# Kernel tuning notes

Measured on AMD Instinct MI355X. Metric: run time of the kernel, lower is better.

## Reference

```python
import jax, jax.numpy as jnp
import numpy as np

N_NODES = 50000
N_EDGES = 500000
IN_DIM = 128
HIDDEN = 32
HEADS = 8
OUT_DIM = HIDDEN * HEADS  # 256
NEG_SLOPE = 0.2


def setup_inputs() -> dict:
    key = jax.random.key(0)
    ks = jax.random.split(key, 10)
    s = lambda fan: 1.0 / np.sqrt(fan)
    x = jax.random.normal(ks[0], (N_NODES, IN_DIM), dtype=jnp.float32)
    edge_index = jax.random.randint(ks[1], (2, N_EDGES), 0, N_NODES, dtype=jnp.int32)
    W1 = jax.random.normal(ks[2], (IN_DIM, HEADS * HIDDEN), jnp.float32) * s(IN_DIM)
    a_src1 = jax.random.normal(ks[3], (HEADS, HIDDEN), jnp.float32) * s(HIDDEN)
    a_dst1 = jax.random.normal(ks[4], (HEADS, HIDDEN), jnp.float32) * s(HIDDEN)
    b1 = jnp.zeros((HEADS * HIDDEN,), jnp.float32)
    W2 = jax.random.normal(ks[5], (OUT_DIM, OUT_DIM), jnp.float32) * s(OUT_DIM)
    a_src2 = jax.random.normal(ks[6], (1, OUT_DIM), jnp.float32) * s(OUT_DIM)
    a_dst2 = jax.random.normal(ks[7], (1, OUT_DIM), jnp.float32) * s(OUT_DIM)
    b2 = jnp.zeros((OUT_DIM,), jnp.float32)
    return {"x": x, "edge_index": edge_index, "W1": W1, "a_src1": a_src1,
            "a_dst1": a_dst1, "b1": b1, "W2": W2, "a_src2": a_src2,
            "a_dst2": a_dst2, "b2": b2}


def _gat_layer(x, src, dst, W, a_src, a_dst, b, heads, ch, concat):
    N = x.shape[0]
    h = (x @ W).reshape(N, heads, ch)                      # [N,H,C]
    e_src = jnp.sum(h * a_src[None], axis=-1)              # [N,H]
    e_dst = jnp.sum(h * a_dst[None], axis=-1)              # [N,H]
    e = jax.nn.leaky_relu(e_src[src] + e_dst[dst], NEG_SLOPE)  # [E,H]
    # softmax over incoming edges of each destination node
    m = jax.ops.segment_max(e, dst, num_segments=N)        # [N,H]
    e = jnp.exp(e - m[dst])
    denom = jax.ops.segment_sum(e, dst, num_segments=N)    # [N,H]
    alpha = e / (denom[dst] + 1e-16)                       # [E,H]
    msg = h[src] * alpha[:, :, None]                       # [E,H,C]
    out = jax.ops.segment_sum(msg, dst, num_segments=N)    # [N,H,C]
    out = out.reshape(N, heads * ch) if concat else out.mean(axis=1)
    return out + b


def reference(x, edge_index, W1, a_src1, a_dst1, b1, W2, a_src2, a_dst2, b2):
    N = x.shape[0]
    # add self loops (PyG GATConv default)
    loops = jnp.arange(N, dtype=edge_index.dtype)
    src = jnp.concatenate([edge_index[0], loops])
    dst = jnp.concatenate([edge_index[1], loops])
    # dropout is identity in eval mode
    h = _gat_layer(x, src, dst, W1, a_src1, a_dst1, b1, HEADS, HIDDEN, True)
    h = jax.nn.elu(h)
    out = _gat_layer(h, src, dst, W2, a_src2, a_dst2, b2, 1, OUT_DIM, False)
    return out
```

## Files before the change

kernel.cpp:

```cpp
#include <hip/hip_runtime.h>
#include <math.h>

#define N_NODES 50000
#define E_ORIG  500000
#define E_TOT   550000
#define NB      196

typedef _Float16 half8 __attribute__((ext_vector_type(8)));
typedef _Float16 half4 __attribute__((ext_vector_type(4)));
typedef float    v4f   __attribute__((ext_vector_type(4)));

__global__ void k_count(const int* __restrict__ ei, int* __restrict__ deg) {
    int e = blockIdx.x * blockDim.x + threadIdx.x;
    if (e >= E_TOT) return;
    int d = (e < E_ORIG) ? ei[E_ORIG + e] : (e - E_ORIG);
    atomicAdd(&deg[d], 1);
}

__global__ __launch_bounds__(256) void k_blocksum(const int* __restrict__ deg,
                                                  int* __restrict__ bsum) {
    int t = threadIdx.x;
    int i = blockIdx.x * 256 + t;
    int v = (i < N_NODES) ? deg[i] : 0;
#pragma unroll
    for (int mk = 1; mk < 64; mk <<= 1) v += __shfl_xor(v, mk, 64);
    __shared__ int ws[4];
    if ((t & 63) == 0) ws[t >> 6] = v;
    __syncthreads();
    if (t == 0) bsum[blockIdx.x] = ws[0] + ws[1] + ws[2] + ws[3];
}

__global__ __launch_bounds__(256) void k_scanbsum(const int* __restrict__ bsum,
                                                  int* __restrict__ boff) {
    __shared__ int s[256];
    int t = threadIdx.x;
    int v = (t < NB) ? bsum[t] : 0;
    s[t] = v;
    __syncthreads();
    for (int o = 1; o < 256; o <<= 1) {
        int x = (t >= o) ? s[t - o] : 0;
        __syncthreads();
        s[t] += x;
        __syncthreads();
    }
    if (t <= NB) boff[t] = (t == 0) ? 0 : s[t - 1];
}

__global__ __launch_bounds__(256) void k_offsets(const int* __restrict__ deg,
                                                 const int* __restrict__ boff,
                                                 int* __restrict__ offsets,
                                                 int* __restrict__ cur) {
    __shared__ int s[256];
    int t = threadIdx.x;
    int i = blockIdx.x * 256 + t;
    int v = (i < N_NODES) ? deg[i] : 0;
    s[t] = v;
    __syncthreads();
    for (int o = 1; o < 256; o <<= 1) {
        int x = (t >= o) ? s[t - o] : 0;
        __syncthreads();
        s[t] += x;
        __syncthreads();
    }
    int off = boff[blockIdx.x] + s[t] - v;
    if (i <= N_NODES) {
        offsets[i] = off;
        if (i < N_NODES) cur[i] = off;
    }
}

__global__ void k_scatter(const int* __restrict__ ei, int* __restrict__ cur,
                          int* __restrict__ csr_src, int* __restrict__ csr_dst) {
    int e = blockIdx.x * blockDim.x + threadIdx.x;
    if (e >= E_TOT) return;
    int s, d;
    if (e < E_ORIG) { s = ei[e]; d = ei[E_ORIG + e]; }
    else            { s = e - E_ORIG; d = s; }
    int slot = atomicAdd(&cur[d], 1);
    csr_src[slot] = s;
    csr_dst[slot] = d;
}

__global__ void k_prepw(const float* __restrict__ W1, const float* __restrict__ W2,
                        const float* __restrict__ as2, const float* __restrict__ ad2,
                        _Float16* __restrict__ w1t, _Float16* __restrict__ w2t,
                        float* __restrict__ vs2, float* __restrict__ vd2,
                        int* __restrict__ deg) {
    int i = blockIdx.x * blockDim.x + threadIdx.x;
    if (i < 128 * 256) {
        int k = i >> 8, c = i & 255;
        w1t[(size_t)c * 128 + k] = (_Float16)W1[i];
        return;
    }
    int j = i - 128 * 256;
    if (j < 256 * 256) {
        int k = j >> 8, c = j & 255;
        w2t[(size_t)c * 256 + k] = (_Float16)W2[j];
        return;
    }
    j -= 256 * 256;
    if (j < 256) {
        float s = 0.f, d = 0.f;
        for (int c = 0; c < 256; c++) {
            float w = W2[(size_t)j * 256 + c];
            s += w * as2[c];
            d += w * ad2[c];
        }
        vs2[j] = s;
        vd2[j] = d;
        return;
    }
    j -= 256;
    if (j < N_NODES) deg[j] = 0;
}

__global__ __launch_bounds__(256) void k_wts1(
    const int* __restrict__ csr_src, const int* __restrict__ csr_dst,
    const float* __restrict__ es, const float* __restrict__ ed,
    float* __restrict__ w1w) {
    int i = blockIdx.x * blockDim.x + threadIdx.x;
    if (i >= E_TOT * 8) return;
    int e = i >> 3, h = i & 7;
    int s = csr_src[e], d = csr_dst[e];
    float l = es[(size_t)s * 8 + h] + ed[(size_t)d * 8 + h];
    l = l > 0.f ? l : 0.2f * l;
    w1w[i] = __expf(l);
}

__global__ __launch_bounds__(256) void k_wts2(
    const int* __restrict__ csr_src, const int* __restrict__ csr_dst,
    const float* __restrict__ es2, const float* __restrict__ ed2,
    float* __restrict__ w2w) {
    int e = blockIdx.x * blockDim.x + threadIdx.x;
    if (e >= E_TOT) return;
    float l = es2[csr_src[e]] + ed2[csr_dst[e]];
    l = l > 0.f ? l : 0.2f * l;
    w2w[e] = __expf(l);
}

__global__ __launch_bounds__(256) void k_gemm1(
    const float* __restrict__ X, const _Float16* __restrict__ Bt,
    const float* __restrict__ a_s, const float* __restrict__ a_d,
    _Float16* __restrict__ H, float* __restrict__ es, float* __restrict__ ed) {
    int t = threadIdx.x, w = t >> 6, lane = t & 63;
    int quad = lane >> 4, l16 = lane & 15;
    int row0 = blockIdx.x * 32;
    int colbase = w * 64;

    v4f acc[2][4];
#pragma unroll
    for (int i = 0; i < 2; i++)
#pragma unroll
        for (int j = 0; j < 4; j++) acc[i][j] = (v4f){0.f, 0.f, 0.f, 0.f};

    int r0 = row0 + l16;      if (r0 >= N_NODES) r0 = N_NODES - 1;
    int r1 = row0 + 16 + l16; if (r1 >= N_NODES) r1 = N_NODES - 1;
    const float4* a0p = (const float4*)(X + (size_t)r0 * 128) + quad * 2;
    const float4* a1p = (const float4*)(X + (size_t)r1 * 128) + quad * 2;
    const half8* bp[4];
#pragma unroll
    for (int ct = 0; ct < 4; ct++)
        bp[ct] = (const half8*)(Bt + (size_t)(colbase + ct * 16 + l16) * 128 + quad * 8);

#pragma unroll
    for (int kc = 0; kc < 4; kc++) {
        float4 f0 = a0p[kc * 8], f1 = a0p[kc * 8 + 1];
        float4 f2 = a1p[kc * 8], f3 = a1p[kc * 8 + 1];
        half8 av0 = (half8){(_Float16)f0.x, (_Float16)f0.y, (_Float16)f0.z, (_Float16)f0.w,
                            (_Float16)f1.x, (_Float16)f1.y, (_Float16)f1.z, (_Float16)f1.w};
        half8 av1 = (half8){(_Float16)f2.x, (_Float16)f2.y, (_Float16)f2.z, (_Float16)f2.w,
                            (_Float16)f3.x, (_Float16)f3.y, (_Float16)f3.z, (_Float16)f3.w};
#pragma unroll
        for (int ct = 0; ct < 4; ct++) {
            half8 bv = bp[ct][kc * 4];
            acc[0][ct] = __builtin_amdgcn_mfma_f32_16x16x32_f16(av0, bv, acc[0][ct], 0, 0, 0);
            acc[1][ct] = __builtin_amdgcn_mfma_f32_16x16x32_f16(av1, bv, acc[1][ct], 0, 0, 0);
        }
    }

    float asv[4], adv[4];
#pragma unroll
    for (int ct = 0; ct < 4; ct++) {
        asv[ct] = a_s[colbase + ct * 16 + l16];
        adv[ct] = a_d[colbase + ct * 16 + l16];
    }
#pragma unroll
    for (int rt = 0; rt < 2; rt++) {
#pragma unroll
        for (int hp = 0; hp < 2; hp++) {
#pragma unroll
            for (int reg = 0; reg < 4; reg++) {
                float ps = acc[rt][2 * hp][reg] * asv[2 * hp] +
                           acc[rt][2 * hp + 1][reg] * asv[2 * hp + 1];
                float pd = acc[rt][2 * hp][reg] * adv[2 * hp] +
                           acc[rt][2 * hp + 1][reg] * adv[2 * hp + 1];
#pragma unroll
                for (int mk = 1; mk < 16; mk <<= 1) {
                    ps += __shfl_xor(ps, mk, 64);
                    pd += __shfl_xor(pd, mk, 64);
                }
                if (l16 == 0) {
                    int row = row0 + rt * 16 + quad * 4 + reg;
                    if (row < N_NODES) {
                        int head = w * 2 + hp;
                        es[(size_t)row * 8 + head] = ps;
                        ed[(size_t)row * 8 + head] = pd;
                    }
                }
            }
        }
    }

    __shared__ _Float16 SH[32][264];
#pragma unroll
    for (int rt = 0; rt < 2; rt++)
#pragma unroll
        for (int ct = 0; ct < 4; ct++)
#pragma unroll
            for (int reg = 0; reg < 4; reg++)
                SH[rt * 16 + quad * 4 + reg][colbase + ct * 16 + l16] =
                    (_Float16)acc[rt][ct][reg];
    __syncthreads();
#pragma unroll
    for (int j = 0; j < 4; j++) {
        int c = j * 256 + t;
        int row = c >> 5, col8 = c & 31;
        int gr = row0 + row;
        if (gr < N_NODES)
            *(half8*)(H + (size_t)gr * 256 + col8 * 8) = *(const half8*)&SH[row][col8 * 8];
    }
}

__global__ __launch_bounds__(256) void k_gemm2(
    const _Float16* __restrict__ A, const _Float16* __restrict__ Bt,
    const float* __restrict__ bias, float* __restrict__ OUT) {
    int t = threadIdx.x, w = t >> 6, lane = t & 63;
    int quad = lane >> 4, l16 = lane & 15;
    int row0 = blockIdx.x * 32;
    int colbase = w * 64;

    v4f acc[2][4];
#pragma unroll
    for (int i = 0; i < 2; i++)
#pragma unroll
        for (int j = 0; j < 4; j++) acc[i][j] = (v4f){0.f, 0.f, 0.f, 0.f};

    int r0 = row0 + l16;      if (r0 >= N_NODES) r0 = N_NODES - 1;
    int r1 = row0 + 16 + l16; if (r1 >= N_NODES) r1 = N_NODES - 1;
    const half8* a0 = (const half8*)(A + (size_t)r0 * 256 + quad * 8);
    const half8* a1 = (const half8*)(A + (size_t)r1 * 256 + quad * 8);
    const half8* bp[4];
#pragma unroll
    for (int ct = 0; ct < 4; ct++)
        bp[ct] = (const half8*)(Bt + (size_t)(colbase + ct * 16 + l16) * 256 + quad * 8);

#pragma unroll
    for (int kc = 0; kc < 8; kc++) {
        half8 av0 = a0[kc * 4];
        half8 av1 = a1[kc * 4];
#pragma unroll
        for (int ct = 0; ct < 4; ct++) {
            half8 bv = bp[ct][kc * 4];
            acc[0][ct] = __builtin_amdgcn_mfma_f32_16x16x32_f16(av0, bv, acc[0][ct], 0, 0, 0);
            acc[1][ct] = __builtin_amdgcn_mfma_f32_16x16x32_f16(av1, bv, acc[1][ct], 0, 0, 0);
        }
    }

    __shared__ float SF[32][260];
#pragma unroll
    for (int rt = 0; rt < 2; rt++)
#pragma unroll
        for (int ct = 0; ct < 4; ct++)
#pragma unroll
            for (int reg = 0; reg < 4; reg++)
                SF[rt * 16 + quad * 4 + reg][colbase + ct * 16 + l16] = acc[rt][ct][reg];
    __syncthreads();
#pragma unroll
    for (int j = 0; j < 8; j++) {
        int c = j * 256 + t;
        int row = c >> 6, c4 = c & 63;
        int gr = row0 + row;
        if (gr < N_NODES) {
            float4 v = *(const float4*)&SF[row][c4 * 4];
            float4 bb = ((const float4*)bias)[c4];
            float4 o = make_float4(v.x + bb.x, v.y + bb.y, v.z + bb.z, v.w + bb.w);
            *(float4*)(OUT + (size_t)gr * 256 + c4 * 4) = o;
        }
    }
}

__global__ __launch_bounds__(256) void k_agg1(
    const _Float16* __restrict__ H1, const float* __restrict__ w1w,
    const int* __restrict__ offsets, const int* __restrict__ csr_src,
    const float* __restrict__ b1, const float* __restrict__ vs2,
    const float* __restrict__ vd2, _Float16* __restrict__ out1,
    float* __restrict__ es2, float* __restrict__ ed2) {
    int t = threadIdx.x, w = t >> 6, lane = t & 63;
    int n = blockIdx.x * 4 + w;
    int hB = lane >> 3;
    int beg = offsets[n];
    int deg = offsets[n + 1] - beg;

    const char* __restrict__ Hb = (const char*)H1 + lane * 8;
    const float* __restrict__ pw = w1w + (size_t)beg * 8 + hB;
    float a0 = 0.f, a1 = 0.f, a2 = 0.f, a3 = 0.f, den = 0.f;

    for (int base = 0; base < deg; base += 64) {
        int rem = deg - base; if (rem > 64) rem = 64;
        int idx = beg + base + lane;
        if (idx >= E_TOT) idx = E_TOT - 1;
        int sreg = csr_src[idx];
        int i = 0;
        for (; i + 1 < rem; i += 2) {
            int s0 = __shfl(sreg, i);
            int s1 = __shfl(sreg, i + 1);
            float w0 = pw[(base + i) * 8];
            float w1 = pw[(base + i + 1) * 8];
            half4 h0 = *(const half4*)(Hb + ((unsigned)s0 << 9));
            half4 h1 = *(const half4*)(Hb + ((unsigned)s1 << 9));
            a0 += w0 * (float)h0[0]; a1 += w0 * (float)h0[1];
            a2 += w0 * (float)h0[2]; a3 += w0 * (float)h0[3];
            a0 += w1 * (float)h1[0]; a1 += w1 * (float)h1[1];
            a2 += w1 * (float)h1[2]; a3 += w1 * (float)h1[3];
            den += w0 + w1;
        }
        if (i < rem) {
            int s0 = __shfl(sreg, i);
            float w0 = pw[(base + i) * 8];
            half4 h0 = *(const half4*)(Hb + ((unsigned)s0 << 9));
            a0 += w0 * (float)h0[0]; a1 += w0 * (float)h0[1];
            a2 += w0 * (float)h0[2]; a3 += w0 * (float)h0[3];
            den += w0;
        }
    }

    float r = 1.f / (den + 1e-16f);
    float4 bb = ((const float4*)b1)[lane];
    float o0 = a0 * r + bb.x, o1 = a1 * r + bb.y;
    float o2 = a2 * r + bb.z, o3 = a3 * r + bb.w;
    o0 = o0 > 0.f ? o0 : __expf(o0) - 1.f;
    o1 = o1 > 0.f ? o1 : __expf(o1) - 1.f;
    o2 = o2 > 0.f ? o2 : __expf(o2) - 1.f;
    o3 = o3 > 0.f ? o3 : __expf(o3) - 1.f;
    ((half4*)(out1 + (size_t)n * 256))[lane] =
        (half4){(_Float16)o0, (_Float16)o1, (_Float16)o2, (_Float16)o3};

    float4 vs = ((const float4*)vs2)[lane];
    float4 vd = ((const float4*)vd2)[lane];
    float ps = o0 * vs.x + o1 * vs.y + o2 * vs.z + o3 * vs.w;
    float pd = o0 * vd.x + o1 * vd.y + o2 * vd.z + o3 * vd.w;
#pragma unroll
    for (int mk = 1; mk < 64; mk <<= 1) {
        ps += __shfl_xor(ps, mk, 64);
        pd += __shfl_xor(pd, mk, 64);
    }
    if (lane == 0) { es2[n] = ps; ed2[n] = pd; }
}

__global__ __launch_bounds__(256) void k_agg2(
    const _Float16* __restrict__ O1, const float* __restrict__ w2w,
    const int* __restrict__ offsets, const int* __restrict__ csr_src,
    _Float16* __restrict__ xagg) {
    int t = threadIdx.x, w = t >> 6, lane = t & 63;
    int n = blockIdx.x * 4 + w;
    int beg = offsets[n];
    int deg = offsets[n + 1] - beg;

    const char* __restrict__ Ob = (const char*)O1 + lane * 8;
    float a0 = 0.f, a1 = 0.f, a2 = 0.f, a3 = 0.f, den = 0.f;

    for (int base = 0; base < deg; base += 64) {
        int rem = deg - base; if (rem > 64) rem = 64;
        int idx = beg + base + lane;
        if (idx >= E_TOT) idx = E_TOT - 1;
        int sreg = csr_src[idx];
        float wreg = w2w[idx];
        int i = 0;
        for (; i + 1 < rem; i += 2) {
            int s0 = __shfl(sreg, i);
            int s1 = __shfl(sreg, i + 1);
            float w0 = __shfl(wreg, i);
            float w1 = __shfl(wreg, i + 1);
            half4 h0 = *(const half4*)(Ob + ((unsigned)s0 << 9));
            half4 h1 = *(const half4*)(Ob + ((unsigned)s1 << 9));
            a0 += w0 * (float)h0[0]; a1 += w0 * (float)h0[1];
            a2 += w0 * (float)h0[2]; a3 += w0 * (float)h0[3];
            a0 += w1 * (float)h1[0]; a1 += w1 * (float)h1[1];
            a2 += w1 * (float)h1[2]; a3 += w1 * (float)h1[3];
            den += w0 + w1;
        }
        if (i < rem) {
            int s0 = __shfl(sreg, i);
            float w0 = __shfl(wreg, i);
            half4 h0 = *(const half4*)(Ob + ((unsigned)s0 << 9));
            a0 += w0 * (float)h0[0]; a1 += w0 * (float)h0[1];
            a2 += w0 * (float)h0[2]; a3 += w0 * (float)h0[3];
            den += w0;
        }
    }

    float r = 1.f / (den + 1e-16f);
    ((half4*)(xagg + (size_t)n * 256))[lane] =
        (half4){(_Float16)(a0 * r), (_Float16)(a1 * r),
                (_Float16)(a2 * r), (_Float16)(a3 * r)};
}

extern "C" void kernel_launch(void* const* d_in, const int* in_sizes, int n_in,
                              void* d_out, int out_size, void* d_ws, size_t ws_size,
                              hipStream_t stream) {
    const float* x   = (const float*)d_in[0];
    const int*   ei  = (const int*)d_in[1];
    const float* W1  = (const float*)d_in[2];
    const float* as1 = (const float*)d_in[3];
    const float* ad1 = (const float*)d_in[4];
    const float* b1  = (const float*)d_in[5];
    const float* W2  = (const float*)d_in[6];
    const float* as2 = (const float*)d_in[7];
    const float* ad2 = (const float*)d_in[8];
    const float* b2  = (const float*)d_in[9];
    float* out = (float*)d_out;

    char* ws = (char*)d_ws;
    size_t off = 0;
    auto alloc = [&](size_t bytes) {
        void* p = ws + off;
        off = (off + bytes + 255) & ~(size_t)255;
        return p;
    };
    _Float16* h1h     = (_Float16*)alloc((size_t)N_NODES * 256 * 2);
    _Float16* out1h   = (_Float16*)alloc((size_t)N_NODES * 256 * 2);
    _Float16* xagg    = (_Float16*)alloc((size_t)N_NODES * 256 * 2);
    _Float16* w1t     = (_Float16*)alloc((size_t)128 * 256 * 2);
    _Float16* w2t     = (_Float16*)alloc((size_t)256 * 256 * 2);
    float*    es1     = (float*)alloc((size_t)N_NODES * 8 * 4);
    float*    ed1     = (float*)alloc((size_t)N_NODES * 8 * 4);
    float*    es2     = (float*)alloc((size_t)N_NODES * 4);
    float*    ed2     = (float*)alloc((size_t)N_NODES * 4);
    float*    vs2     = (float*)alloc(256 * 4);
    float*    vd2     = (float*)alloc(256 * 4);
    float*    w1w     = (float*)alloc((size_t)E_TOT * 8 * 4);
    float*    w2w     = (float*)alloc((size_t)E_TOT * 4);
    int*      deg     = (int*)alloc((size_t)N_NODES * 4);
    int*      offsets = (int*)alloc((size_t)(N_NODES + 1) * 4);
    int*      cur     = (int*)alloc((size_t)N_NODES * 4);
    int*      csr_src = (int*)alloc((size_t)E_TOT * 4);
    int*      csr_dst = (int*)alloc((size_t)E_TOT * 4);
    int*      bsum    = (int*)alloc((size_t)NB * 4);
    int*      boff    = (int*)alloc((size_t)(NB + 1) * 4);

    const int TB = 256;
    int gridE = (E_TOT + TB - 1) / TB;
    int gridG = (N_NODES + 31) / 32;
    int gridA = N_NODES / 4;

    int prepN = 128 * 256 + 256 * 256 + 256 + N_NODES;
    k_prepw<<<(prepN + TB - 1) / TB, TB, 0, stream>>>(W1, W2, as2, ad2,
                                                      w1t, w2t, vs2, vd2, deg);
    k_count<<<gridE, TB, 0, stream>>>(ei, deg);
    k_blocksum<<<NB, TB, 0, stream>>>(deg, bsum);
    k_scanbsum<<<1, TB, 0, stream>>>(bsum, boff);
    k_offsets<<<NB, TB, 0, stream>>>(deg, boff, offsets, cur);
    k_scatter<<<gridE, TB, 0, stream>>>(ei, cur, csr_src, csr_dst);

    k_gemm1<<<gridG, TB, 0, stream>>>(x, w1t, as1, ad1, h1h, es1, ed1);
    k_wts1<<<(E_TOT * 8 + TB - 1) / TB, TB, 0, stream>>>(csr_src, csr_dst,
                                                         es1, ed1, w1w);
    k_agg1<<<gridA, TB, 0, stream>>>(h1h, w1w, offsets, csr_src, b1,
                                     vs2, vd2, out1h, es2, ed2);

    k_wts2<<<gridE, TB, 0, stream>>>(csr_src, csr_dst, es2, ed2, w2w);
    k_agg2<<<gridA, TB, 0, stream>>>(out1h, w2w, offsets, csr_src, xagg);
    k_gemm2<<<gridG, TB, 0, stream>>>(xagg, w2t, b2, out);
}
```

Measured before the change: 339.4 us.

## Split wavefront into half-waves gathering 16-byte rows in aggregation kernels

The two aggregation kernels now split each wavefront into two 32-lane halves that handle alternate edges. Each lane loads 8 halfs (16 bytes) per neighbor instead of 4, and the two halves' partial sums are combined with a cross-half shuffle at the end. This aims for wider loads and two independent gathers in flight per wave. The GEMM epilogues also stage the output through a 16-row shared buffer in two passes, which halves shared memory use at the cost of an extra barrier.

```diff
diff --git a/kernel.cpp b/kernel.cpp
--- a/kernel.cpp
+++ b/kernel.cpp
@@ -211,23 +211,24 @@
         }
     }
 
-    __shared__ _Float16 SH[32][264];
-#pragma unroll
-    for (int rt = 0; rt < 2; rt++)
+    __shared__ _Float16 SH[16][264];
+#pragma unroll
+    for (int rt = 0; rt < 2; rt++) {
+        if (rt) __syncthreads();
 #pragma unroll
         for (int ct = 0; ct < 4; ct++)
 #pragma unroll
             for (int reg = 0; reg < 4; reg++)
-                SH[rt * 16 + quad * 4 + reg][colbase + ct * 16 + l16] =
-                    (_Float16)acc[rt][ct][reg];
-    __syncthreads();
-#pragma unroll
-    for (int j = 0; j < 4; j++) {
-        int c = j * 256 + t;
-        int row = c >> 5, col8 = c & 31;
-        int gr = row0 + row;
-        if (gr < N_NODES)
-            *(half8*)(H + (size_t)gr * 256 + col8 * 8) = *(const half8*)&SH[row][col8 * 8];
+                SH[quad * 4 + reg][colbase + ct * 16 + l16] = (_Float16)acc[rt][ct][reg];
+        __syncthreads();
+#pragma unroll
+        for (int j = 0; j < 2; j++) {
+            int c = j * 256 + t;
+            int row = c >> 5, col8 = c & 31;
+            int gr = row0 + rt * 16 + row;
+            if (gr < N_NODES)
+                *(half8*)(H + (size_t)gr * 256 + col8 * 8) = *(const half8*)&SH[row][col8 * 8];
+        }
     }
 }
 
@@ -266,25 +267,27 @@
         }
     }
 
-    __shared__ float SF[32][260];
-#pragma unroll
-    for (int rt = 0; rt < 2; rt++)
+    __shared__ float SF[16][260];
+#pragma unroll
+    for (int rt = 0; rt < 2; rt++) {
+        if (rt) __syncthreads();
 #pragma unroll
         for (int ct = 0; ct < 4; ct++)
 #pragma unroll
             for (int reg = 0; reg < 4; reg++)
-                SF[rt * 16 + quad * 4 + reg][colbase + ct * 16 + l16] = acc[rt][ct][reg];
-    __syncthreads();
-#pragma unroll
-    for (int j = 0; j < 8; j++) {
-        int c = j * 256 + t;
-        int row = c >> 6, c4 = c & 63;
-        int gr = row0 + row;
-        if (gr < N_NODES) {
-            float4 v = *(const float4*)&SF[row][c4 * 4];
-            float4 bb = ((const float4*)bias)[c4];
-            float4 o = make_float4(v.x + bb.x, v.y + bb.y, v.z + bb.z, v.w + bb.w);
-            *(float4*)(OUT + (size_t)gr * 256 + c4 * 4) = o;
+                SF[quad * 4 + reg][colbase + ct * 16 + l16] = acc[rt][ct][reg];
+        __syncthreads();
+#pragma unroll
+        for (int j = 0; j < 4; j++) {
+            int c = j * 256 + t;
+            int row = c >> 6, c4 = c & 63;
+            int gr = row0 + rt * 16 + row;
+            if (gr < N_NODES) {
+                float4 v = *(const float4*)&SF[row][c4 * 4];
+                float4 bb = ((const float4*)bias)[c4];
+                float4 o = make_float4(v.x + bb.x, v.y + bb.y, v.z + bb.z, v.w + bb.w);
+                *(float4*)(OUT + (size_t)gr * 256 + c4 * 4) = o;
+            }
         }
     }
 }
@@ -297,60 +300,71 @@
     float* __restrict__ es2, float* __restrict__ ed2) {
     int t = threadIdx.x, w = t >> 6, lane = t & 63;
     int n = blockIdx.x * 4 + w;
-    int hB = lane >> 3;
+    int half = lane >> 5;
+    int c8 = lane & 31;
+    int hB = c8 >> 2;
     int beg = offsets[n];
     int deg = offsets[n + 1] - beg;
 
-    const char* __restrict__ Hb = (const char*)H1 + lane * 8;
+    const char* __restrict__ Hb = (const char*)H1 + c8 * 16;
     const float* __restrict__ pw = w1w + (size_t)beg * 8 + hB;
-    float a0 = 0.f, a1 = 0.f, a2 = 0.f, a3 = 0.f, den = 0.f;
+    float a0 = 0.f, a1 = 0.f, a2 = 0.f, a3 = 0.f;
+    float a4 = 0.f, a5 = 0.f, a6 = 0.f, a7 = 0.f, den = 0.f;
 
     for (int base = 0; base < deg; base += 64) {
         int rem = deg - base; if (rem > 64) rem = 64;
         int idx = beg + base + lane;
         if (idx >= E_TOT) idx = E_TOT - 1;
         int sreg = csr_src[idx];
-        int i = 0;
-        for (; i + 1 < rem; i += 2) {
-            int s0 = __shfl(sreg, i);
-            int s1 = __shfl(sreg, i + 1);
-            float w0 = pw[(base + i) * 8];
-            float w1 = pw[(base + i + 1) * 8];
-            half4 h0 = *(const half4*)(Hb + ((unsigned)s0 << 9));
-            half4 h1 = *(const half4*)(Hb + ((unsigned)s1 << 9));
-            a0 += w0 * (float)h0[0]; a1 += w0 * (float)h0[1];
-            a2 += w0 * (float)h0[2]; a3 += w0 * (float)h0[3];
-            a0 += w1 * (float)h1[0]; a1 += w1 * (float)h1[1];
-            a2 += w1 * (float)h1[2]; a3 += w1 * (float)h1[3];
-            den += w0 + w1;
-        }
-        if (i < rem) {
+        for (int i = half; i < rem; i += 2) {
             int s0 = __shfl(sreg, i);
             float w0 = pw[(base + i) * 8];
-            half4 h0 = *(const half4*)(Hb + ((unsigned)s0 << 9));
-            a0 += w0 * (float)h0[0]; a1 += w0 * (float)h0[1];
-            a2 += w0 * (float)h0[2]; a3 += w0 * (float)h0[3];
+            half8 h = *(const half8*)(Hb + ((size_t)(unsigned)s0 << 9));
+            a0 += w0 * (float)h[0]; a1 += w0 * (float)h[1];
+            a2 += w0 * (float)h[2]; a3 += w0 * (float)h[3];
+            a4 += w0 * (float)h[4]; a5 += w0 * (float)h[5];
+            a6 += w0 * (float)h[6]; a7 += w0 * (float)h[7];
             den += w0;
         }
     }
 
+    a0 += __shfl_xor(a0, 32, 64); a1 += __shfl_xor(a1, 32, 64);
+    a2 += __shfl_xor(a2, 32, 64); a3 += __shfl_xor(a3, 32, 64);
+    a4 += __shfl_xor(a4, 32, 64); a5 += __shfl_xor(a5, 32, 64);
+    a6 += __shfl_xor(a6, 32, 64); a7 += __shfl_xor(a7, 32, 64);
+    den += __shfl_xor(den, 32, 64);
+
     float r = 1.f / (den + 1e-16f);
-    float4 bb = ((const float4*)b1)[lane];
-    float o0 = a0 * r + bb.x, o1 = a1 * r + bb.y;
-    float o2 = a2 * r + bb.z, o3 = a3 * r + bb.w;
+    float4 bl = ((const float4*)b1)[c8 * 2];
+    float4 bh = ((const float4*)b1)[c8 * 2 + 1];
+    float o0 = a0 * r + bl.x, o1 = a1 * r + bl.y;
+    float o2 = a2 * r + bl.z, o3 = a3 * r + bl.w;
+    float o4 = a4 * r + bh.x, o5 = a5 * r + bh.y;
+    float o6 = a6 * r + bh.z, o7 = a7 * r + bh.w;
     o0 = o0 > 0.f ? o0 : __expf(o0) - 1.f;
     o1 = o1 > 0.f ? o1 : __expf(o1) - 1.f;
     o2 = o2 > 0.f ? o2 : __expf(o2) - 1.f;
     o3 = o3 > 0.f ? o3 : __expf(o3) - 1.f;
-    ((half4*)(out1 + (size_t)n * 256))[lane] =
-        (half4){(_Float16)o0, (_Float16)o1, (_Float16)o2, (_Float16)o3};
-
-    float4 vs = ((const float4*)vs2)[lane];
-    float4 vd = ((const float4*)vd2)[lane];
-    float ps = o0 * vs.x + o1 * vs.y + o2 * vs.z + o3 * vs.w;
-    float pd = o0 * vd.x + o1 * vd.y + o2 * vd.z + o3 * vd.w;
-#pragma unroll
-    for (int mk = 1; mk < 64; mk <<= 1) {
+    o4 = o4 > 0.f ? o4 : __expf(o4) - 1.f;
+    o5 = o5 > 0.f ? o5 : __expf(o5) - 1.f;
+    o6 = o6 > 0.f ? o6 : __expf(o6) - 1.f;
+    o7 = o7 > 0.f ? o7 : __expf(o7) - 1.f;
+    if (half == 0) {
+        half8 hv = (half8){(_Float16)o0, (_Float16)o1, (_Float16)o2, (_Float16)o3,
+                           (_Float16)o4, (_Float16)o5, (_Float16)o6, (_Float16)o7};
+        *((half8*)(out1 + (size_t)n * 256) + c8) = hv;
+    }
+
+    float4 vsl = ((const float4*)vs2)[c8 * 2];
+    float4 vsh = ((const float4*)vs2)[c8 * 2 + 1];
+    float4 vdl = ((const float4*)vd2)[c8 * 2];
+    float4 vdh = ((const float4*)vd2)[c8 * 2 + 1];
+    float ps = o0 * vsl.x + o1 * vsl.y + o2 * vsl.z + o3 * vsl.w +
+               o4 * vsh.x + o5 * vsh.y + o6 * vsh.z + o7 * vsh.w;
+    float pd = o0 * vdl.x + o1 * vdl.y + o2 * vdl.z + o3 * vdl.w +
+               o4 * vdh.x + o5 * vdh.y + o6 * vdh.z + o7 * vdh.w;
+#pragma unroll
+    for (int mk = 1; mk < 32; mk <<= 1) {
         ps += __shfl_xor(ps, mk, 64);
         pd += __shfl_xor(pd, mk, 64);
     }
@@ -363,11 +377,13 @@
     _Float16* __restrict__ xagg) {
     int t = threadIdx.x, w = t >> 6, lane = t & 63;
     int n = blockIdx.x * 4 + w;
+    int half = lane >> 5, c8 = lane & 31;
     int beg = offsets[n];
     int deg = offsets[n + 1] - beg;
 
-    const char* __restrict__ Ob = (const char*)O1 + lane * 8;
-    float a0 = 0.f, a1 = 0.f, a2 = 0.f, a3 = 0.f, den = 0.f;
+    const char* __restrict__ Ob = (const char*)O1 + c8 * 16;
+    float a0 = 0.f, a1 = 0.f, a2 = 0.f, a3 = 0.f;
+    float a4 = 0.f, a5 = 0.f, a6 = 0.f, a7 = 0.f, den = 0.f;
 
     for (int base = 0; base < deg; base += 64) {
         int rem = deg - base; if (rem > 64) rem = 64;
@@ -375,34 +391,32 @@
         if (idx >= E_TOT) idx = E_TOT - 1;
         int sreg = csr_src[idx];
         float wreg = w2w[idx];
-        int i = 0;
-        for (; i + 1 < rem; i += 2) {
-            int s0 = __shfl(sreg, i);
-            int s1 = __shfl(sreg, i + 1);
-            float w0 = __shfl(wreg, i);
-            float w1 = __shfl(wreg, i + 1);
-            half4 h0 = *(const half4*)(Ob + ((unsigned)s0 << 9));
-            half4 h1 = *(const half4*)(Ob + ((unsigned)s1 << 9));
-            a0 += w0 * (float)h0[0]; a1 += w0 * (float)h0[1];
-            a2 += w0 * (float)h0[2]; a3 += w0 * (float)h0[3];
-            a0 += w1 * (float)h1[0]; a1 += w1 * (float)h1[1];
-            a2 += w1 * (float)h1[2]; a3 += w1 * (float)h1[3];
-            den += w0 + w1;
-        }
-        if (i < rem) {
+        for (int i = half; i < rem; i += 2) {
             int s0 = __shfl(sreg, i);
             float w0 = __shfl(wreg, i);
-            half4 h0 = *(const half4*)(Ob + ((unsigned)s0 << 9));
-            a0 += w0 * (float)h0[0]; a1 += w0 * (float)h0[1];
-            a2 += w0 * (float)h0[2]; a3 += w0 * (float)h0[3];
+            half8 h = *(const half8*)(Ob + ((size_t)(unsigned)s0 << 9));
+            a0 += w0 * (float)h[0]; a1 += w0 * (float)h[1];
+            a2 += w0 * (float)h[2]; a3 += w0 * (float)h[3];
+            a4 += w0 * (float)h[4]; a5 += w0 * (float)h[5];
+            a6 += w0 * (float)h[6]; a7 += w0 * (float)h[7];
             den += w0;
         }
     }
 
+    a0 += __shfl_xor(a0, 32, 64); a1 += __shfl_xor(a1, 32, 64);
+    a2 += __shfl_xor(a2, 32, 64); a3 += __shfl_xor(a3, 32, 64);
+    a4 += __shfl_xor(a4, 32, 64); a5 += __shfl_xor(a5, 32, 64);
+    a6 += __shfl_xor(a6, 32, 64); a7 += __shfl_xor(a7, 32, 64);
+    den += __shfl_xor(den, 32, 64);
+
     float r = 1.f / (den + 1e-16f);
-    ((half4*)(xagg + (size_t)n * 256))[lane] =
-        (half4){(_Float16)(a0 * r), (_Float16)(a1 * r),
-                (_Float16)(a2 * r), (_Float16)(a3 * r)};
+    if (half == 0) {
+        half8 hv = (half8){(_Float16)(a0 * r), (_Float16)(a1 * r),
+                           (_Float16)(a2 * r), (_Float16)(a3 * r),
+                           (_Float16)(a4 * r), (_Float16)(a5 * r),
+                           (_Float16)(a6 * r), (_Float16)(a7 * r)};
+        *((half8*)(xagg + (size_t)n * 256) + c8) = hv;
+    }
 }
 
 extern "C" void kernel_launch(void* const* d_in, const int* in_sizes, int n_in,
```

Measured after the change: 342.9 us. About the same (+1.0%).
